# Performance work log

Hardware: AMD Instinct MI355X
Metric: run time of the kernel (lower is better)

The kernel has to match this reference:

```python
import jax, jax.numpy as jnp
import numpy as np

N, C, T, V = 64, 64, 256, 25
R, O = C // 8, 64  # rel_channels, out_channels
ALPHA = 1.0


def setup_inputs() -> dict:
    key = jax.random.key(0)
    ks = jax.random.split(key, 10)
    s = 0.05
    return {
        "x": jax.random.normal(ks[0], (N, C, T, V), dtype=jnp.float32),
        "A": jax.random.normal(ks[1], (V, V), dtype=jnp.float32),
        "w1": jax.random.normal(ks[2], (R, C), dtype=jnp.float32) * s,
        "b1": jnp.zeros((R,), dtype=jnp.float32),
        "w2": jax.random.normal(ks[3], (R, C), dtype=jnp.float32) * s,
        "b2": jnp.zeros((R,), dtype=jnp.float32),
        "w3": jax.random.normal(ks[4], (O, C), dtype=jnp.float32) * s,
        "b3": jnp.zeros((O,), dtype=jnp.float32),
        "w4": jax.random.normal(ks[5], (O, R), dtype=jnp.float32) * s,
        "b4": jnp.zeros((O,), dtype=jnp.float32),
    }


def reference(x, A, w1, b1, w2, b2, w3, b3, w4, b4):
    # x: (N, C, T, V)
    # conv1/conv2 are 1x1 convs followed by mean over T -> (N, R, V)
    x1 = jnp.einsum('nctv,rc->nrv', x, w1) / x.shape[2] + b1[:, None]
    x2 = jnp.einsum('nctv,rc->nrv', x, w2) / x.shape[2] + b2[:, None]
    # conv3: 1x1 conv -> (N, O, T, V)
    x3 = jnp.einsum('nctv,oc->notv', x, w3) + b3[:, None, None]
    # outer-difference attention over joints: (N, R, V, V)
    att = jnp.tanh(x1[:, :, :, None] - x2[:, :, None, :])
    # conv4 channel mix (R->O), scale, add adjacency: (N, O, V, V)
    m = jnp.einsum('nruv,or->nouv', att, w4) + b4[:, None, None]
    m = m * ALPHA + A[None, None, :, :]
    # aggregation: einsum('ncuv,nctv->nctu')
    out = jnp.einsum('ncuv,nctv->nctu', m, x3)
    return out
```

## Files before the change

### kernel.cpp

```cpp
#include <hip/hip_runtime.h>

#define NN 64
#define CC 64
#define TT 256
#define VV 25
#define RR 8
#define OO 64
#define PLANE 6400
#define SX 101


__global__ __launch_bounds__(256) void k_xsum(const float* __restrict__ x,
                                              float* __restrict__ xsum,
                                              const float* __restrict__ w3,
                                              float* __restrict__ w3t) {
  int nc = blockIdx.x;
  int tid = threadIdx.x;
  if (blockIdx.x < 16) {
    int k = blockIdx.x * 256 + tid;
    int c = k >> 6, o = k & 63;
    w3t[k] = w3[o * 64 + c];
  }
  const float4* src4 = (const float4*)(x + (size_t)nc * PLANE);
  __shared__ __align__(16) float s[PLANE + 256];
  float4* s4 = (float4*)s;
  for (int k = tid; k < PLANE / 4; k += 256) s4[k] = src4[k];
  __syncthreads();
  if (tid < 200) {
    int tg = tid / 25, v = tid - tg * 25;
    float a0 = 0.f, a1 = 0.f, a2 = 0.f, a3 = 0.f;
    for (int k = 0; k < 32; k += 4) {
      a0 += s[(tg + 8 * (k + 0)) * VV + v];
      a1 += s[(tg + 8 * (k + 1)) * VV + v];
      a2 += s[(tg + 8 * (k + 2)) * VV + v];
      a3 += s[(tg + 8 * (k + 3)) * VV + v];
    }
    s[PLANE + tid] = (a0 + a1) + (a2 + a3);
  }
  __syncthreads();
  if (tid < VV) {
    float a = 0.f;
#pragma unroll
    for (int g = 0; g < 8; ++g) a += s[PLANE + g * VV + tid];
    xsum[nc * VV + tid] = a;
  }
}

__global__ __launch_bounds__(256) void k_build_m(
    const float* __restrict__ xsum, const float* __restrict__ A,
    const float* __restrict__ w1, const float* __restrict__ b1,
    const float* __restrict__ w2, const float* __restrict__ b2,
    const float* __restrict__ w4, const float* __restrict__ b4,
    float* __restrict__ mp) {
  int n = blockIdx.x;
  int og = blockIdx.y;
  __shared__ float xs[CC * VV];
  __shared__ float sx1[RR * VV];
  __shared__ float sx2[RR * VV];
  __shared__ float att[RR * 625];
  int tid = threadIdx.x;
  const float* xsn = xsum + n * (CC * VV);
  for (int k = tid; k < CC * VV; k += 256) xs[k] = xsn[k];
  __syncthreads();
  if (tid < RR * VV) {
    int r = tid / VV, v = tid % VV;
    float a1 = 0.f, a2 = 0.f;
#pragma unroll
    for (int c = 0; c < CC; ++c) {
      float xv = xs[c * VV + v];
      a1 = fmaf(w1[r * CC + c], xv, a1);
      a2 = fmaf(w2[r * CC + c], xv, a2);
    }
    sx1[tid] = a1 * (1.f / 256.f) + b1[r];
    sx2[tid] = a2 * (1.f / 256.f) + b2[r];
  }
  __syncthreads();
  for (int k = tid; k < RR * 625; k += 256) {
    int r = k / 625, uv = k % 625;
    int u = uv / VV, v = uv % VV;
    att[k] = tanhf(sx1[r * VV + u] - sx2[r * VV + v]);
  }
  __syncthreads();
  for (int k = tid; k < 8 * 625; k += 256) {
    int o = og * 8 + k / 625, vu = k % 625;
    int v = vu / VV, u = vu % VV;
    float a = b4[o] + A[u * VV + v];
#pragma unroll
    for (int r = 0; r < RR; ++r)
      a = fmaf(w4[o * RR + r], att[r * 625 + u * VV + v], a);
    mp[(((size_t)n * OO + o) * VV + v) * 32 + u] = a;
  }
}

template <int O0>
__device__ __forceinline__ void conv_half(const float* __restrict__ xb,
                                          const float* __restrict__ w3t,
                                          const float* __restrict__ b3,
                                          float* __restrict__ s) {
  int p = threadIdx.x & 127;
  if (p >= 100) return;
  const float* xp = xb + p;
  float acc[32];
#pragma unroll
  for (int o = 0; o < 32; ++o) acc[o] = b3[O0 + o];
  for (int c = 0; c < CC; c += 8) {
    float xv[8];
#pragma unroll
    for (int j = 0; j < 8; ++j) xv[j] = xp[(size_t)(c + j) * PLANE];
#pragma unroll
    for (int j = 0; j < 8; ++j) {
      const float* w = w3t + (c + j) * OO + O0;
#pragma unroll
      for (int o = 0; o < 32; ++o) acc[o] = fmaf(w[o], xv[j], acc[o]);
    }
  }
#pragma unroll
  for (int o = 0; o < 32; ++o) s[(O0 + o) * SX + p] = acc[o];
}

__global__ __launch_bounds__(256, 6) void k_fused(
    const float* __restrict__ x, const float* __restrict__ w3t,
    const float* __restrict__ b3, const float* __restrict__ mp,
    float* __restrict__ out) {
  int n = blockIdx.y;
  int t0 = blockIdx.x * 4;
  __shared__ float s[OO * SX];
  int tid = threadIdx.x;

  const float* xb = x + (size_t)n * CC * PLANE + t0 * VV;
  if (tid < 128)
    conv_half<0>(xb, w3t, b3, s);
  else
    conv_half<32>(xb, w3t, b3, s);
  __syncthreads();

  {
    int o = tid >> 2, uq = tid & 3;
    const float* mb = mp + (size_t)(n * OO + o) * (VV * 32) + uq * 8;
    const float* xr = s + o * SX;
    float acc[4][8];
#pragma unroll
    for (int t = 0; t < 4; ++t)
#pragma unroll
      for (int j = 0; j < 8; ++j) acc[t][j] = 0.f;
#pragma unroll 2
    for (int v = 0; v < VV; ++v) {
      float4 m0 = *(const float4*)(mb + v * 32);
      float4 m1 = *(const float4*)(mb + v * 32 + 4);
      float xt[4];
#pragma unroll
      for (int t = 0; t < 4; ++t) xt[t] = xr[t * VV + v];
#pragma unroll
      for (int t = 0; t < 4; ++t) {
        acc[t][0] = fmaf(m0.x, xt[t], acc[t][0]);
        acc[t][1] = fmaf(m0.y, xt[t], acc[t][1]);
        acc[t][2] = fmaf(m0.z, xt[t], acc[t][2]);
        acc[t][3] = fmaf(m0.w, xt[t], acc[t][3]);
        acc[t][4] = fmaf(m1.x, xt[t], acc[t][4]);
        acc[t][5] = fmaf(m1.y, xt[t], acc[t][5]);
        acc[t][6] = fmaf(m1.z, xt[t], acc[t][6]);
        acc[t][7] = fmaf(m1.w, xt[t], acc[t][7]);
      }
    }
    __syncthreads();
#pragma unroll
    for (int t = 0; t < 4; ++t)
#pragma unroll
      for (int j = 0; j < 8; ++j) {
        int u = uq * 8 + j;
        if (u < VV) s[o * SX + t * VV + u] = acc[t][j];
      }
  }
  __syncthreads();

  float* ob = out + (size_t)n * OO * PLANE + t0 * VV;
  for (int k = tid; k < OO * 100; k += 256) {
    int oo = k / 100, p = k - oo * 100;
    ob[(size_t)oo * PLANE + p] = s[oo * SX + p];
  }
}

extern "C" void kernel_launch(void* const* d_in, const int* in_sizes, int n_in,
                              void* d_out, int out_size, void* d_ws,
                              size_t ws_size, hipStream_t stream) {
  const float* x = (const float*)d_in[0];
  const float* A = (const float*)d_in[1];
  const float* w1 = (const float*)d_in[2];
  const float* b1 = (const float*)d_in[3];
  const float* w2 = (const float*)d_in[4];
  const float* b2 = (const float*)d_in[5];
  const float* w3 = (const float*)d_in[6];
  const float* b3 = (const float*)d_in[7];
  const float* w4 = (const float*)d_in[8];
  const float* b4 = (const float*)d_in[9];
  float* out = (float*)d_out;
  float* ws = (float*)d_ws;

  float* xsum = ws;
  float* w3t = ws + 102400;
  float* mp = ws + 106496;

  k_xsum<<<NN * CC, 256, 0, stream>>>(x, xsum, w3, w3t);
  k_build_m<<<dim3(NN, 8), 256, 0, stream>>>(xsum, A, w1, b1, w2, b2, w4, b4,
                                             mp);
  k_fused<<<dim3(TT / 4, NN), 256, 0, stream>>>(x, w3t, b3, mp, out);
}
```

Measured before the change: 305.0 us.

## Compute 1x1 conv3 with fp16 MFMA and fold bias into aggregation

```diff
diff --git a/kernel.cpp b/kernel.cpp
--- a/kernel.cpp
+++ b/kernel.cpp
@@ -8,18 +8,21 @@
 #define OO 64
 #define PLANE 6400
 #define SX 101
-
+#define MPS 832
+
+
+typedef _Float16 f16x8 __attribute__((ext_vector_type(8)));
+typedef float f32x16 __attribute__((ext_vector_type(16)));
 
 __global__ __launch_bounds__(256) void k_xsum(const float* __restrict__ x,
                                               float* __restrict__ xsum,
                                               const float* __restrict__ w3,
-                                              float* __restrict__ w3t) {
+                                              _Float16* __restrict__ w3h) {
   int nc = blockIdx.x;
   int tid = threadIdx.x;
   if (blockIdx.x < 16) {
     int k = blockIdx.x * 256 + tid;
-    int c = k >> 6, o = k & 63;
-    w3t[k] = w3[o * 64 + c];
+    w3h[k] = (_Float16)w3[k];
   }
   const float4* src4 = (const float4*)(x + (size_t)nc * PLANE);
   __shared__ __align__(16) float s[PLANE + 256];
@@ -50,8 +53,8 @@
     const float* __restrict__ xsum, const float* __restrict__ A,
     const float* __restrict__ w1, const float* __restrict__ b1,
     const float* __restrict__ w2, const float* __restrict__ b2,
-    const float* __restrict__ w4, const float* __restrict__ b4,
-    float* __restrict__ mp) {
+    const float* __restrict__ b3, const float* __restrict__ w4,
+    const float* __restrict__ b4, float* __restrict__ mp) {
   int n = blockIdx.x;
   int og = blockIdx.y;
   __shared__ float xs[CC * VV];
@@ -88,61 +91,76 @@
 #pragma unroll
     for (int r = 0; r < RR; ++r)
       a = fmaf(w4[o * RR + r], att[r * 625 + u * VV + v], a);
-    mp[(((size_t)n * OO + o) * VV + v) * 32 + u] = a;
-  }
-}
-
-template <int O0>
-__device__ __forceinline__ void conv_half(const float* __restrict__ xb,
-                                          const float* __restrict__ w3t,
-                                          const float* __restrict__ b3,
-                                          float* __restrict__ s) {
-  int p = threadIdx.x & 127;
-  if (p >= 100) return;
-  const float* xp = xb + p;
-  float acc[32];
-#pragma unroll
-  for (int o = 0; o < 32; ++o) acc[o] = b3[O0 + o];
-  for (int c = 0; c < CC; c += 8) {
-    float xv[8];
-#pragma unroll
-    for (int j = 0; j < 8; ++j) xv[j] = xp[(size_t)(c + j) * PLANE];
-#pragma unroll
-    for (int j = 0; j < 8; ++j) {
-      const float* w = w3t + (c + j) * OO + O0;
-#pragma unroll
-      for (int o = 0; o < 32; ++o) acc[o] = fmaf(w[o], xv[j], acc[o]);
-    }
-  }
-#pragma unroll
-  for (int o = 0; o < 32; ++o) s[(O0 + o) * SX + p] = acc[o];
+    mp[(size_t)(n * OO + o) * MPS + v * 32 + u] = a;
+  }
+  __syncthreads();
+  if (tid < 200) {
+    int ol = tid / 25, u = tid % 25;
+    int o = og * 8 + ol;
+    const float* row = mp + (size_t)(n * OO + o) * MPS;
+    float sum = 0.f;
+#pragma unroll
+    for (int v = 0; v < VV; ++v) sum += row[v * 32 + u];
+    mp[(size_t)(n * OO + o) * MPS + 800 + u] = b3[o] * sum;
+  }
 }
 
 __global__ __launch_bounds__(256, 6) void k_fused(
-    const float* __restrict__ x, const float* __restrict__ w3t,
-    const float* __restrict__ b3, const float* __restrict__ mp,
-    float* __restrict__ out) {
+    const float* __restrict__ x, const _Float16* __restrict__ w3h,
+    const float* __restrict__ mp, float* __restrict__ out) {
   int n = blockIdx.y;
   int t0 = blockIdx.x * 4;
   __shared__ float s[OO * SX];
   int tid = threadIdx.x;
 
-  const float* xb = x + (size_t)n * CC * PLANE + t0 * VV;
-  if (tid < 128)
-    conv_half<0>(xb, w3t, b3, s);
-  else
-    conv_half<32>(xb, w3t, b3, s);
+  {
+    int lane = tid & 63;
+    int pt = tid >> 6;
+    int p = pt * 32 + (lane & 31);
+    int pc = p < 100 ? p : 99;
+    int chalf = (lane >> 5) * 8;
+    const float* xb = x + (size_t)n * CC * PLANE + t0 * VV + pc;
+    const _Float16* wa0 = w3h + (lane & 31) * 64 + chalf;
+    const _Float16* wa1 = w3h + ((lane & 31) + 32) * 64 + chalf;
+    f32x16 acc0 = {0, 0, 0, 0, 0, 0, 0, 0, 0, 0, 0, 0, 0, 0, 0, 0};
+    f32x16 acc1 = {0, 0, 0, 0, 0, 0, 0, 0, 0, 0, 0, 0, 0, 0, 0, 0};
+#pragma unroll 2
+    for (int ks = 0; ks < 4; ++ks) {
+      float xv[8];
+#pragma unroll
+      for (int e = 0; e < 8; ++e)
+        xv[e] = xb[(size_t)(ks * 16 + chalf + e) * PLANE];
+      f16x8 bf;
+#pragma unroll
+      for (int e = 0; e < 8; ++e) bf[e] = (_Float16)xv[e];
+      f16x8 a0 = *(const f16x8*)(wa0 + ks * 16);
+      f16x8 a1 = *(const f16x8*)(wa1 + ks * 16);
+      acc0 = __builtin_amdgcn_mfma_f32_32x32x16_f16(a0, bf, acc0, 0, 0, 0);
+      acc1 = __builtin_amdgcn_mfma_f32_32x32x16_f16(a1, bf, acc1, 0, 0, 0);
+    }
+    if (p < 100) {
+#pragma unroll
+      for (int r = 0; r < 16; ++r) {
+        int row = (r & 3) + 8 * (r >> 2) + 4 * (lane >> 5);
+        s[row * SX + p] = acc0[r];
+        s[(row + 32) * SX + p] = acc1[r];
+      }
+    }
+  }
   __syncthreads();
 
   {
     int o = tid >> 2, uq = tid & 3;
-    const float* mb = mp + (size_t)(n * OO + o) * (VV * 32) + uq * 8;
+    const float* mb = mp + (size_t)(n * OO + o) * MPS + uq * 8;
     const float* xr = s + o * SX;
+    float4 i0 = *(const float4*)(mb + 800);
+    float4 i1 = *(const float4*)(mb + 804);
     float acc[4][8];
 #pragma unroll
-    for (int t = 0; t < 4; ++t)
-#pragma unroll
-      for (int j = 0; j < 8; ++j) acc[t][j] = 0.f;
+    for (int t = 0; t < 4; ++t) {
+      acc[t][0] = i0.x; acc[t][1] = i0.y; acc[t][2] = i0.z; acc[t][3] = i0.w;
+      acc[t][4] = i1.x; acc[t][5] = i1.y; acc[t][6] = i1.z; acc[t][7] = i1.w;
+    }
 #pragma unroll 2
     for (int v = 0; v < VV; ++v) {
       float4 m0 = *(const float4*)(mb + v * 32);
@@ -197,11 +215,11 @@
   float* ws = (float*)d_ws;
 
   float* xsum = ws;
-  float* w3t = ws + 102400;
-  float* mp = ws + 106496;
-
-  k_xsum<<<NN * CC, 256, 0, stream>>>(x, xsum, w3, w3t);
-  k_build_m<<<dim3(NN, 8), 256, 0, stream>>>(xsum, A, w1, b1, w2, b2, w4, b4,
-                                             mp);
-  k_fused<<<dim3(TT / 4, NN), 256, 0, stream>>>(x, w3t, b3, mp, out);
-}
+  _Float16* w3h = (_Float16*)(ws + 102400);
+  float* mp = ws + 102400 + 2048;
+
+  k_xsum<<<NN * CC, 256, 0, stream>>>(x, xsum, w3, w3h);
+  k_build_m<<<dim3(NN, 8), 256, 0, stream>>>(xsum, A, w1, b1, w2, b2, b3, w4,
+                                             b4, mp);
+  k_fused<<<dim3(TT / 4, NN), 256, 0, stream>>>(x, w3h, mp, out);
+}
```

New measurement: 293.4 us. 1.04x faster.
